# Optimization experiments

Hardware: AMD Instinct MI355X
Metric: run time of the kernel (lower is better)

Reference implementation:

```python
import jax, jax.numpy as jnp
import numpy as np

EPS = 0.0001
N_NODES = 8192
N_GRAPHS = 128
NODES_PER_G = 64
N_FEAT = 128
CLDIM = 512
LAYERS = 3
HEADS = 8
HID = 64
N_EDGES = 262144
N_CLASSES = 10


def setup_inputs():
    key = jax.random.key(0)
    ks = jax.random.split(key, 12)
    x = jax.random.normal(ks[0], (N_NODES, N_FEAT), jnp.float32)

    def rand_edges(k):
        k1, k2 = jax.random.split(k)
        g = jax.random.randint(k1, (N_EDGES,), 0, N_GRAPHS)
        loc = jax.random.randint(k2, (2, N_EDGES), 0, NODES_PER_G)
        return (g[None, :] * NODES_PER_G + loc).astype(jnp.int32)

    edge_index = rand_edges(ks[1])
    neg_edge_index = rand_edges(ks[2])
    batch = (jnp.arange(N_NODES) // NODES_PER_G).astype(jnp.int32)
    # mask indices: all within-graph node pairs (block-diagonal mask==1)
    base = jnp.arange(N_GRAPHS) * NODES_PER_G
    a = jnp.repeat(jnp.arange(NODES_PER_G), NODES_PER_G)
    b = jnp.tile(jnp.arange(NODES_PER_G), NODES_PER_G)
    midx = jnp.stack([
        (base[:, None] + a[None, :]).reshape(-1),
        (base[:, None] + b[None, :]).reshape(-1),
    ]).astype(jnp.int32)
    s = 0.05
    return dict(
        x=x, edge_index=edge_index, neg_edge_index=neg_edge_index,
        batch=batch, midx=midx,
        fc_W=jax.random.normal(ks[3], (N_FEAT, CLDIM), jnp.float32) * s,
        fc_b=jnp.zeros((CLDIM,), jnp.float32),
        bn_g=jnp.ones((LAYERS, CLDIM), jnp.float32),
        bn_b=jnp.zeros((LAYERS, CLDIM), jnp.float32),
        conv_W=jax.random.normal(ks[4], (LAYERS, CLDIM, CLDIM), jnp.float32) * s,
        conv_b=jnp.zeros((LAYERS, CLDIM), jnp.float32),
        feat_W=jax.random.normal(ks[5], (LAYERS * CLDIM, HEADS * HID), jnp.float32) * s,
        phi=jax.random.normal(ks[6], (HEADS, 2 * HID, 1), jnp.float32) * s,
        fc1_W=jax.random.normal(ks[7], (HEADS * HID, HID), jnp.float32) * s,
        fc1_b=jnp.zeros((HID,), jnp.float32),
        fc2_W=jax.random.normal(ks[8], (HID, N_CLASSES), jnp.float32) * s,
        fc2_b=jnp.zeros((N_CLASSES,), jnp.float32),
    )


def _bn(h, g, b):
    # BatchNorm1d in training mode (biased variance over nodes)
    m = jnp.mean(h, 0)
    v = jnp.var(h, 0)
    return (h - m) * jax.lax.rsqrt(v + 1e-5) * g + b


def _gcn(h, W, b, src, dst, n):
    # GCNConv with added self-loops: D^-1/2 (A+I) D^-1/2 (h W) + b
    h2 = h @ W
    deg = jax.ops.segment_sum(jnp.ones(src.shape[0], h.dtype), dst, n) + 1.0
    dinv = jax.lax.rsqrt(deg)
    coef = (dinv[src] * dinv[dst])[:, None]
    agg = jax.ops.segment_sum(h2[src] * coef, dst, n)
    return agg + h2 / deg[:, None] + b


def _forward(x, fc_W, fc_b, bn_g, bn_b, conv_W, conv_b, feat_W, phi,
             fc1_W, fc1_b, fc2_W, fc2_b, edge_index, neg_edge_index, batch, midx):
    n = x.shape[0]
    h = x @ fc_W + fc_b
    src, dst = edge_index[0], edge_index[1]
    hs = []
    for i in range(LAYERS):
        h = _bn(h, bn_g[i], bn_b[i])
        h = jax.nn.relu(_gcn(h, conv_W[i], conv_b[i], src, dst, n))
        hs.append(h)
    z = jnp.concatenate(hs, -1)  # [N, LAYERS*CLDIM]

    # ---- recon loss: per-edge inner-product decoder, mean-pooled per graph ----
    def edge_loss(ei, neg):
        v = jnp.sum(z[ei[0]] * z[ei[1]], -1)
        sgm = jax.nn.sigmoid(v)
        l = -jnp.log(EPS + (1.0 - sgm if neg else sgm))
        seg = batch[ei[0]]
        cnt = jax.ops.segment_sum(jnp.ones_like(l), seg, N_GRAPHS)
        tot = jax.ops.segment_sum(l, seg, N_GRAPHS)
        return jnp.sum(tot / jnp.maximum(cnt, 1.0))

    Lrc = (edge_loss(edge_index, False) + edge_loss(neg_edge_index, True)) / N_GRAPHS

    # ---- classifier: multi-head sigmoid attention over mask pairs ----
    xh = (z @ feat_W).reshape(n, HEADS, HID)
    phi_a = phi[:, :HID, 0]   # [H, HID]
    phi_b = phi[:, HID:, 0]   # [H, HID]
    # cat([x_i, x_j]) @ phi == x_i @ phi_a + x_j @ phi_b, computed per node then gathered
    s1 = jnp.einsum('nhd,hd->nh', xh, phi_a)
    s2 = jnp.einsum('nhd,hd->nh', xh, phi_b)
    w = jax.nn.sigmoid(jax.nn.leaky_relu(s1[midx[0]] + s2[midx[1]]))  # [M, H]
    msg = (xh[midx[1]] * w[:, :, None]).reshape(-1, HEADS * HID)      # [M, H*HID]
    agg = jax.ops.segment_sum(msg, midx[0], n)
    logits = jax.nn.leaky_relu(agg @ fc1_W + fc1_b) @ fc2_W + fc2_b
    tmp = jnp.exp(logits - jnp.max(logits, -1, keepdims=True)) + EPS
    preds = tmp / jnp.sum(tmp, -1, keepdims=True)
    cnt = jax.ops.segment_sum(jnp.ones((n,), preds.dtype), batch, N_GRAPHS)
    yp = jax.ops.segment_sum(preds, batch, N_GRAPHS) / cnt[:, None]
    return jnp.log(yp), Lrc, preds


def reference(x, edge_index, neg_edge_index, batch, midx, fc_W, fc_b, bn_g, bn_b,
              conv_W, conv_b, feat_W, phi, fc1_W, fc1_b, fc2_W, fc2_b):
    return _forward(x, fc_W, fc_b, bn_g, bn_b, conv_W, conv_b, feat_W, phi,
                    fc1_W, fc1_b, fc2_W, fc2_b, edge_index, neg_edge_index, batch, midx)
```

## Files before the change

kernel.cpp:

```cpp
#include <hip/hip_runtime.h>

#define NN 8192
#define NG 128
#define NF 128
#define CL 512
#define ZD 1536
#define NE 262144

typedef __attribute__((ext_vector_type(8))) _Float16 half8;
typedef __attribute__((ext_vector_type(4))) float f32x4;

__global__ void deg_kernel(const int* __restrict__ dst, float* __restrict__ deg) {
    int e = blockIdx.x * 256 + threadIdx.x;
    atomicAdd(&deg[dst[e]], 1.0f);
}

__global__ void build_adj(const int* __restrict__ src, const int* __restrict__ dst,
                          const float* __restrict__ deg, float* __restrict__ A) {
    int e = blockIdx.x * 256 + threadIdx.x;
    int s = src[e], d = dst[e];
    int g = d >> 6;
    float w = rsqrtf(deg[s] + 1.0f) * rsqrtf(deg[d] + 1.0f);
    atomicAdd(&A[(size_t)((g << 6) + (d & 63)) * 64 + (s & 63)], w);
}

__global__ void cvtA(const float* __restrict__ Amat, const float* __restrict__ deg,
                     _Float16* __restrict__ Ah) {
    int t = blockIdx.x * 256 + threadIdx.x;
    int i4 = t * 4;
    int g = i4 >> 12, loc = i4 & 4095;
    float4 v = *(const float4*)(Amat + (size_t)g * 4096 + loc);
    float vv[4] = {v.x, v.y, v.z, v.w};
    int row = loc >> 6;
    int c0 = loc & 63;
    int ed = row - c0;
    if (ed >= 0 && ed < 4) vv[ed] += 1.0f / (deg[g * 64 + row] + 1.0f);
    int swz = (row & 7) << 3;
    #pragma unroll
    for (int e = 0; e < 4; ++e)
        Ah[(size_t)g * 4096 + ((loc + e) ^ swz)] = (_Float16)vv[e];
}

__global__ void cvt_h(const float* __restrict__ in, _Float16* __restrict__ out) {
    int i = blockIdx.x * 256 + threadIdx.x;
    float4 a = *(const float4*)(in + (size_t)i * 8);
    float4 b = *(const float4*)(in + (size_t)i * 8 + 4);
    half8 o;
    o[0] = (_Float16)a.x; o[1] = (_Float16)a.y; o[2] = (_Float16)a.z; o[3] = (_Float16)a.w;
    o[4] = (_Float16)b.x; o[5] = (_Float16)b.y; o[6] = (_Float16)b.z; o[7] = (_Float16)b.w;
    *(half8*)(out + (size_t)i * 8) = o;
}

__global__ void cvtT(const float* __restrict__ W, _Float16* __restrict__ Wt,
                     int Kd, int Nd) {
    __shared__ float t[32][33];
    int kb = blockIdx.y * 32, nb = blockIdx.x * 32;
    int tx = threadIdx.x, ty = threadIdx.y;
    for (int i = ty; i < 32; i += 8)
        t[i][tx] = W[(size_t)(kb + i) * Nd + nb + tx];
    __syncthreads();
    for (int i = ty; i < 32; i += 8)
        Wt[(size_t)(nb + i) * Kd + kb + tx] = (_Float16)t[tx][i];
}

__global__ void wprep(const float* __restrict__ W,
                      const float* __restrict__ sums, const float* __restrict__ sqs,
                      const float* __restrict__ g, const float* __restrict__ b,
                      _Float16* __restrict__ Wt, float* __restrict__ bias2,
                      int Kd, int Nd) {
    __shared__ float t[32][33];
    __shared__ float tks[32];
    int kb = blockIdx.y * 32, nb = blockIdx.x * 32;
    int tx = threadIdx.x, ty = threadIdx.y;
    for (int i = ty; i < 32; i += 8)
        t[i][tx] = W[(size_t)(kb + i) * Nd + nb + tx];
    int kc = kb + tx;
    float m = sums[kc] * (1.0f / NN);
    float var = sqs[kc] * (1.0f / NN) - m * m;
    float sc = rsqrtf(var + 1e-5f) * g[kc];
    if (ty == 0) tks[tx] = b[kc] - m * sc;
    __syncthreads();
    for (int i = ty; i < 32; i += 8)
        Wt[(size_t)(nb + i) * Kd + kb + tx] = (_Float16)(t[tx][i] * sc);
    if (ty == 0) {
        float acc = 0.f;
        #pragma unroll
        for (int i = 0; i < 32; ++i) acc = fmaf(tks[i], t[i][tx], acc);
        atomicAdd(&bias2[nb + tx], acc);
    }
}

template<int ACT, bool HASB, bool OUT16, bool STATS, bool FUSE>
__global__ __launch_bounds__(256)
void gemm_f16(const _Float16* __restrict__ A, int lda,
              const _Float16* __restrict__ Bt, int ldb,
              float* __restrict__ Cf, _Float16* __restrict__ Ch, int ldc,
              const float* __restrict__ bias, int K,
              float* __restrict__ sums, float* __restrict__ sqs,
              const _Float16* __restrict__ Ahg,
              const float* __restrict__ cb,
              _Float16* __restrict__ Zout)
{
    __shared__ __align__(16) char SMraw[FUSE ? 34816 : 24576];
    _Float16* As = (_Float16*)SMraw;
    _Float16* Bs = (_Float16*)(SMraw + 16384);
    const int tid = threadIdx.x;
    const int lane = tid & 63, wave = tid >> 6;
    const int wr = wave >> 1, wc = wave & 1;
    const int ntile = gridDim.x;
    const int li = blockIdx.y * ntile + blockIdx.x;
    const int x8 = li & 7, rest = li >> 3;
    const int bt = rest % ntile;
    const int bp = (rest / ntile) * 8 + x8;
    const int bm = bp * 128, bn = bt * 64;

    f32x4 acc[4][2];
    #pragma unroll
    for (int m = 0; m < 4; ++m)
        #pragma unroll
        for (int n = 0; n < 2; ++n)
            acc[m][n] = (f32x4){0.f, 0.f, 0.f, 0.f};

    const int fl = lane & 15, kh = (lane >> 4) * 8;
    const int sw = (fl & 7) << 3;

    for (int k0 = 0; k0 < K; k0 += 64) {
        #pragma unroll
        for (int j = 0; j < 4; ++j) {
            int d = wave * 2048 + j * 512 + lane * 8;
            int row = d >> 6, kk = d & 63;
            int sk = kk ^ ((row & 7) << 3);
            __builtin_amdgcn_global_load_lds(
                (const __attribute__((address_space(1))) void*)(A + (size_t)(bm + row) * lda + k0 + sk),
                (__attribute__((address_space(3))) void*)&As[wave * 2048 + j * 512], 16, 0, 0);
        }
        #pragma unroll
        for (int j = 0; j < 2; ++j) {
            int d = wave * 1024 + j * 512 + lane * 8;
            int row = d >> 6, kk = d & 63;
            int sk = kk ^ ((row & 7) << 3);
            __builtin_amdgcn_global_load_lds(
                (const __attribute__((address_space(1))) void*)(Bt + (size_t)(bn + row) * ldb + k0 + sk),
                (__attribute__((address_space(3))) void*)&Bs[wave * 1024 + j * 512], 16, 0, 0);
        }
        __syncthreads();
        #pragma unroll
        for (int kc = 0; kc < 2; ++kc) {
            int ko = (kc * 32 + kh) ^ sw;
            half8 av[4], bv[2];
            #pragma unroll
            for (int m = 0; m < 4; ++m)
                av[m] = *(const half8*)&As[(wr * 64 + m * 16 + fl) * 64 + ko];
            #pragma unroll
            for (int n = 0; n < 2; ++n)
                bv[n] = *(const half8*)&Bs[(wc * 32 + n * 16 + fl) * 64 + ko];
            #pragma unroll
            for (int m = 0; m < 4; ++m)
                #pragma unroll
                for (int n = 0; n < 2; ++n)
                    acc[m][n] = __builtin_amdgcn_mfma_f32_16x16x32_f16(av[m], bv[n], acc[m][n], 0, 0, 0);
        }
        __syncthreads();
    }

    const int orow0 = (lane >> 4) * 4;
    const int ocol  = lane & 15;

    if constexpr (!FUSE) {
        #pragma unroll
        for (int n = 0; n < 2; ++n) {
            int col = bn + wc * 32 + n * 16 + ocol;
            float bb = HASB ? bias[col] : 0.f;
            float ss = 0.f, qq = 0.f;
            #pragma unroll
            for (int m = 0; m < 4; ++m) {
                #pragma unroll
                for (int r = 0; r < 4; ++r) {
                    int rowg = bm + wr * 64 + m * 16 + orow0 + r;
                    float v = acc[m][n][r] + bb;
                    if (ACT == 2) v = v > 0.f ? v : 0.01f * v;
                    if (STATS) { ss += v; qq = fmaf(v, v, qq); }
                    if (OUT16) Ch[(size_t)rowg * ldc + col] = (_Float16)v;
                    else       Cf[(size_t)rowg * ldc + col] = v;
                }
            }
            if (STATS) {
                ss += __shfl_down(ss, 32); ss += __shfl_down(ss, 16);
                qq += __shfl_down(qq, 32); qq += __shfl_down(qq, 16);
                if (lane < 16) {
                    atomicAdd(&sums[col], ss);
                    atomicAdd(&sqs[col], qq);
                }
            }
        }
    } else {
        _Float16* AsA = (_Float16*)SMraw;
        _Float16* Xs  = (_Float16*)(SMraw + 16384);
        const _Float16* Ag = Ahg + (size_t)(bm >> 6) * 4096;
        #pragma unroll
        for (int j = 0; j < 4; ++j)
            __builtin_amdgcn_global_load_lds(
                (const __attribute__((address_space(1))) void*)(Ag + wave * 2048 + j * 512 + lane * 8),
                (__attribute__((address_space(3))) void*)&AsA[wave * 2048 + j * 512], 16, 0, 0);
        #pragma unroll
        for (int n = 0; n < 2; ++n) {
            int c = wc * 32 + n * 16 + ocol;
            float bb = HASB ? bias[bn + c] : 0.f;
            int csw = (c & 7) << 3;
            #pragma unroll
            for (int m = 0; m < 4; ++m) {
                #pragma unroll
                for (int r = 0; r < 4; ++r) {
                    int srow = wr * 64 + m * 16 + orow0 + r;
                    Xs[c * 128 + (srow & 64) + ((srow & 63) ^ csw)] = (_Float16)(acc[m][n][r] + bb);
                }
            }
        }
        __syncthreads();
        const int gg = wave >> 1, rh = wave & 1;
        f32x4 acc2[2][4];
        #pragma unroll
        for (int m2 = 0; m2 < 2; ++m2)
            #pragma unroll
            for (int n2 = 0; n2 < 4; ++n2)
                acc2[m2][n2] = (f32x4){0.f, 0.f, 0.f, 0.f};
        #pragma unroll
        for (int kc = 0; kc < 2; ++kc) {
            int ko = (kc * 32 + kh) ^ sw;
            #pragma unroll
            for (int m2 = 0; m2 < 2; ++m2) {
                int arow = rh * 32 + m2 * 16 + fl;
                half8 av = *(const half8*)&AsA[gg * 4096 + arow * 64 + ko];
                #pragma unroll
                for (int n2 = 0; n2 < 4; ++n2) {
                    int c = n2 * 16 + fl;
                    half8 bv = *(const half8*)&Xs[c * 128 + gg * 64 + ((kc * 32 + kh) ^ ((c & 7) << 3))];
                    acc2[m2][n2] = __builtin_amdgcn_mfma_f32_16x16x32_f16(av, bv, acc2[m2][n2], 0, 0, 0);
                }
            }
        }
        __syncthreads();
        float* Cs = (float*)SMraw;
        #pragma unroll
        for (int m2 = 0; m2 < 2; ++m2)
            #pragma unroll
            for (int n2 = 0; n2 < 4; ++n2)
                #pragma unroll
                for (int r = 0; r < 4; ++r)
                    Cs[(gg * 64 + rh * 32 + m2 * 16 + orow0 + r) * 68 + n2 * 16 + ocol] = acc2[m2][n2][r];
        __syncthreads();
        const int rr = tid >> 3, dq = tid & 7;
        #pragma unroll
        for (int pass = 0; pass < 4; ++pass) {
            int row = pass * 32 + rr;
            half8 hv;
            #pragma unroll
            for (int e = 0; e < 8; ++e) {
                float v = Cs[row * 68 + dq * 8 + e] + cb[bn + dq * 8 + e];
                v = v > 0.f ? v : 0.f;
                hv[e] = (_Float16)v;
            }
            *(half8*)(Zout + (size_t)(bm + row) * ZD + bn + dq * 8) = hv;
        }
        if (STATS && tid < 64) {
            float bb = cb[bn + tid];
            float ss = 0.f, qq = 0.f;
            for (int row = 0; row < 128; ++row) {
                float v = Cs[row * 68 + tid] + bb;
                v = v > 0.f ? v : 0.f;
                ss += v;
                qq = fmaf(v, v, qq);
            }
            atomicAdd(&sums[bn + tid], ss);
            atomicAdd(&sqs[bn + tid], qq);
        }
    }
}

__global__ __launch_bounds__(256)
void gram_mfma(const _Float16* __restrict__ Z, float* __restrict__ Gparts)
{
    __shared__ _Float16 Zs[4096];
    const int g = blockIdx.x, khalf = blockIdx.y;
    const int tid = threadIdx.x;
    const int lane = tid & 63, wave = tid >> 6;
    const int fl = lane & 15, kh = (lane >> 4) * 8;
    const int sw = (fl & 7) << 3;
    float* G = Gparts + (size_t)khalf * NG * 4096;

    f32x4 acc[4];
    #pragma unroll
    for (int n = 0; n < 4; ++n) acc[n] = (f32x4){0.f, 0.f, 0.f, 0.f};

    for (int k0 = khalf * (ZD / 2); k0 < (khalf + 1) * (ZD / 2); k0 += 64) {
        #pragma unroll
        for (int j = 0; j < 2; ++j) {
            int d = wave * 1024 + j * 512 + lane * 8;
            int row = d >> 6, kk = d & 63;
            int sk = kk ^ ((row & 7) << 3);
            __builtin_amdgcn_global_load_lds(
                (const __attribute__((address_space(1))) void*)(Z + (size_t)(g * 64 + row) * ZD + k0 + sk),
                (__attribute__((address_space(3))) void*)&Zs[wave * 1024 + j * 512], 16, 0, 0);
        }
        __syncthreads();
        #pragma unroll
        for (int kc = 0; kc < 2; ++kc) {
            int ko = (kc * 32 + kh) ^ sw;
            half8 av = *(const half8*)&Zs[(wave * 16 + fl) * 64 + ko];
            #pragma unroll
            for (int n = 0; n < 4; ++n) {
                half8 bv = *(const half8*)&Zs[(n * 16 + fl) * 64 + ko];
                acc[n] = __builtin_amdgcn_mfma_f32_16x16x32_f16(av, bv, acc[n], 0, 0, 0);
            }
        }
        __syncthreads();
    }
    const int orow0 = (lane >> 4) * 4;
    const int ocol  = lane & 15;
    #pragma unroll
    for (int n = 0; n < 4; ++n)
        #pragma unroll
        for (int r = 0; r < 4; ++r)
            G[(size_t)(g * 64 + wave * 16 + orow0 + r) * 64 + n * 16 + ocol] = acc[n][r];
}

__global__ void edge_loss2(const int* __restrict__ ei, const int* __restrict__ nei,
                           const float* __restrict__ G0, float* __restrict__ LOSS)
{
    const int setid = blockIdx.y;
    const int* e0 = setid ? nei : ei;
    const int* e1 = e0 + NE;
    float* tot = LOSS + setid * 256;
    float* cnt = tot + 128;
    const float* G1 = G0 + (size_t)NG * 4096;
    __shared__ float lt[128];
    __shared__ float lc[128];
    int tid = threadIdx.x;
    if (tid < 128) { lt[tid] = 0.f; lc[tid] = 0.f; }
    __syncthreads();
    for (int e = blockIdx.x * blockDim.x + tid; e < NE; e += gridDim.x * blockDim.x) {
        int a = e0[e], b = e1[e];
        int g = a >> 6;
        size_t idx = (size_t)((g << 6) + (a & 63)) * 64 + (b & 63);
        float v = G0[idx] + G1[idx];
        float s = 1.f / (1.f + expf(-v));
        float p = setid ? (1.f - s) : s;
        float l = -logf(1e-4f + p);
        atomicAdd(&lt[g], l);
        atomicAdd(&lc[g], 1.f);
    }
    __syncthreads();
    if (tid < 128) {
        atomicAdd(&tot[tid], lt[tid]);
        atomicAdd(&cnt[tid], lc[tid]);
    }
}

__global__ void lrc_final(const float* __restrict__ loss, float* __restrict__ out)
{
    int t = threadIdx.x;
    float v = loss[t] / fmaxf(loss[128 + t], 1.f) + loss[256 + t] / fmaxf(loss[384 + t], 1.f);
    __shared__ float red[128];
    red[t] = v;
    __syncthreads();
    for (int s = 64; s; s >>= 1) {
        if (t < s) red[t] += red[t + s];
        __syncthreads();
    }
    if (t == 0) out[0] = red[0] * (1.0f / 128.0f);
}

__global__ __launch_bounds__(256)
void featattn(const _Float16* __restrict__ Z, const _Float16* __restrict__ featWt,
              const float* __restrict__ phi, _Float16* __restrict__ agg)
{
    __shared__ __align__(16) char SMraw[68608];
    _Float16* As  = (_Float16*)SMraw;
    _Float16* Bs  = (_Float16*)(SMraw + 16384);
    float*    Cs  = (float*)SMraw;
    _Float16* Xt  = (_Float16*)(SMraw + 34816);
    _Float16* Ws  = (_Float16*)(SMraw + 51200);
    float*    s1s = (float*)(SMraw + 67584);
    float*    s2s = (float*)(SMraw + 68096);
    const int pnl = blockIdx.x, h = blockIdx.y;
    const int bm = pnl * 128;
    const int tid = threadIdx.x;
    const int lane = tid & 63, wave = tid >> 6;
    const int wr = wave >> 1, wc = wave & 1;
    const int fl = lane & 15, kh = (lane >> 4) * 8;
    const int sw = (fl & 7) << 3;

    f32x4 acc[4][2];
    #pragma unroll
    for (int m = 0; m < 4; ++m)
        #pragma unroll
        for (int n = 0; n < 2; ++n)
            acc[m][n] = (f32x4){0.f, 0.f, 0.f, 0.f};

    for (int k0 = 0; k0 < ZD; k0 += 64) {
        #pragma unroll
        for (int j = 0; j < 4; ++j) {
            int d = wave * 2048 + j * 512 + lane * 8;
            int row = d >> 6, kk = d & 63;
            int sk = kk ^ ((row & 7) << 3);
            __builtin_amdgcn_global_load_lds(
                (const __attribute__((address_space(1))) void*)(Z + (size_t)(bm + row) * ZD + k0 + sk),
                (__attribute__((address_space(3))) void*)&As[wave * 2048 + j * 512], 16, 0, 0);
        }
        #pragma unroll
        for (int j = 0; j < 2; ++j) {
            int d = wave * 1024 + j * 512 + lane * 8;
            int row = d >> 6, kk = d & 63;
            int sk = kk ^ ((row & 7) << 3);
            __builtin_amdgcn_global_load_lds(
                (const __attribute__((address_space(1))) void*)(featWt + (size_t)(h * 64 + row) * ZD + k0 + sk),
                (__attribute__((address_space(3))) void*)&Bs[wave * 1024 + j * 512], 16, 0, 0);
        }
        __syncthreads();
        #pragma unroll
        for (int kc = 0; kc < 2; ++kc) {
            int ko = (kc * 32 + kh) ^ sw;
            half8 av[4], bv[2];
            #pragma unroll
            for (int m = 0; m < 4; ++m)
                av[m] = *(const half8*)&As[(wr * 64 + m * 16 + fl) * 64 + ko];
            #pragma unroll
            for (int n = 0; n < 2; ++n)
                bv[n] = *(const half8*)&Bs[(wc * 32 + n * 16 + fl) * 64 + ko];
            #pragma unroll
            for (int m = 0; m < 4; ++m)
                #pragma unroll
                for (int n = 0; n < 2; ++n)
                    acc[m][n] = __builtin_amdgcn_mfma_f32_16x16x32_f16(av[m], bv[n], acc[m][n], 0, 0, 0);
        }
        __syncthreads();
    }
    const int orow0 = (lane >> 4) * 4, ocol = lane & 15;
    #pragma unroll
    for (int n = 0; n < 2; ++n) {
        int col = wc * 32 + n * 16 + ocol;
        #pragma unroll
        for (int m = 0; m < 4; ++m)
            #pragma unroll
            for (int r = 0; r < 4; ++r)
                Cs[(wr * 64 + m * 16 + orow0 + r) * 68 + col] = acc[m][n][r];
    }
    __syncthreads();
    {
        const int bnode = tid >> 1, dq = tid & 1;
        const int gg = bnode >> 6, bloc = bnode & 63;
        const float* pa = phi + h * 128 + dq * 32;
        const float* pb = pa + 64;
        float sa = 0.f, sb = 0.f;
        #pragma unroll
        for (int j = 0; j < 32; ++j) {
            int d = dq * 32 + j;
            float vf = Cs[bnode * 68 + d];
            Xt[gg * 4096 + ((d * 64 + bloc) ^ ((d & 7) << 3))] = (_Float16)vf;
            sa = fmaf(vf, pa[j], sa);
            sb = fmaf(vf, pb[j], sb);
        }
        sa += __shfl_down(sa, 1);
        sb += __shfl_down(sb, 1);
        if (dq == 0) { s1s[bnode] = sa; s2s[bnode] = sb; }
    }
    __syncthreads();
    {
        const int inode = tid >> 1, bq = tid & 1;
        const int gg = inode >> 6, iloc = inode & 63;
        float si = s1s[inode];
        #pragma unroll
        for (int e = 0; e < 32; ++e) {
            int b = bq * 32 + e;
            float t = si + s2s[gg * 64 + b];
            t = t > 0.f ? t : 0.01f * t;
            float w = 1.f / (1.f + expf(-t));
            Ws[gg * 4096 + ((iloc * 64 + b) ^ ((iloc & 7) << 3))] = (_Float16)w;
        }
    }
    __syncthreads();
    const int gg = wave >> 1, rh = wave & 1;
    f32x4 acc2[2][4];
    #pragma unroll
    for (int m2 = 0; m2 < 2; ++m2)
        #pragma unroll
        for (int n2 = 0; n2 < 4; ++n2)
            acc2[m2][n2] = (f32x4){0.f, 0.f, 0.f, 0.f};
    #pragma unroll
    for (int kc = 0; kc < 2; ++kc) {
        #pragma unroll
        for (int m2 = 0; m2 < 2; ++m2) {
            int arow = rh * 32 + m2 * 16 + fl;
            half8 av = *(const half8*)&Ws[gg * 4096 + ((arow * 64 + kc * 32 + kh) ^ ((arow & 7) << 3))];
            #pragma unroll
            for (int n2 = 0; n2 < 4; ++n2) {
                int rowb = n2 * 16 + fl;
                half8 bv = *(const half8*)&Xt[gg * 4096 + ((rowb * 64 + kc * 32 + kh) ^ ((rowb & 7) << 3))];
                acc2[m2][n2] = __builtin_amdgcn_mfma_f32_16x16x32_f16(av, bv, acc2[m2][n2], 0, 0, 0);
            }
        }
    }
    __syncthreads();
    #pragma unroll
    for (int m2 = 0; m2 < 2; ++m2)
        #pragma unroll
        for (int n2 = 0; n2 < 4; ++n2)
            #pragma unroll
            for (int r = 0; r < 4; ++r)
                Cs[(gg * 64 + rh * 32 + m2 * 16 + orow0 + r) * 68 + n2 * 16 + ocol] = acc2[m2][n2][r];
    __syncthreads();
    {
        const int rr = tid >> 3, dq = tid & 7;
        #pragma unroll
        for (int pass = 0; pass < 4; ++pass) {
            int row = pass * 32 + rr;
            half8 hv;
            #pragma unroll
            for (int e = 0; e < 8; ++e)
                hv[e] = (_Float16)Cs[row * 68 + dq * 8 + e];
            *(half8*)(agg + (size_t)(bm + row) * CL + h * 64 + dq * 8) = hv;
        }
    }
}

__global__ __launch_bounds__(256)
void fc1head(const _Float16* __restrict__ AGG, const _Float16* __restrict__ fc1Wt,
             const float* __restrict__ fc1b,
             const float* __restrict__ fc2W, const float* __restrict__ fc2b,
             float* __restrict__ preds, float* __restrict__ outlog)
{
    __shared__ __align__(16) char SMraw[17664];
    _Float16* As = (_Float16*)SMraw;
    _Float16* Bs = (_Float16*)(SMraw + 8192);
    float*    Cs = (float*)SMraw;
    const int g = blockIdx.x;
    const int tid = threadIdx.x;
    const int lane = tid & 63, wave = tid >> 6;
    const int fl = lane & 15, kh = (lane >> 4) * 8;
    const int sw = (fl & 7) << 3;

    f32x4 acc[4];
    #pragma unroll
    for (int n = 0; n < 4; ++n) acc[n] = (f32x4){0.f, 0.f, 0.f, 0.f};

    for (int k0 = 0; k0 < CL; k0 += 64) {
        #pragma unroll
        for (int j = 0; j < 2; ++j) {
            int d = wave * 1024 + j * 512 + lane * 8;
            int row = d >> 6, kk = d & 63;
            int sk = kk ^ ((row & 7) << 3);
            __builtin_amdgcn_global_load_lds(
                (const __attribute__((address_space(1))) void*)(AGG + (size_t)(g * 64 + row) * CL + k0 + sk),
                (__attribute__((address_space(3))) void*)&As[wave * 1024 + j * 512], 16, 0, 0);
            __builtin_amdgcn_global_load_lds(
                (const __attribute__((address_space(1))) void*)(fc1Wt + (size_t)row * CL + k0 + sk),
                (__attribute__((address_space(3))) void*)&Bs[wave * 1024 + j * 512], 16, 0, 0);
        }
        __syncthreads();
        #pragma unroll
        for (int kc = 0; kc < 2; ++kc) {
            int ko = (kc * 32 + kh) ^ sw;
            half8 av = *(const half8*)&As[(wave * 16 + fl) * 64 + ko];
            #pragma unroll
            for (int n = 0; n < 4; ++n) {
                half8 bv = *(const half8*)&Bs[(n * 16 + fl) * 64 + ko];
                acc[n] = __builtin_amdgcn_mfma_f32_16x16x32_f16(av, bv, acc[n], 0, 0, 0);
            }
        }
        __syncthreads();
    }
    const int orow0 = (lane >> 4) * 4, ocol = lane & 15;
    #pragma unroll
    for (int n = 0; n < 4; ++n) {
        int col = n * 16 + ocol;
        float bb = fc1b[col];
        #pragma unroll
        for (int r = 0; r < 4; ++r) {
            float v = acc[n][r] + bb;
            v = v > 0.f ? v : 0.01f * v;
            Cs[(wave * 16 + orow0 + r) * 69 + col] = v;
        }
    }
    __syncthreads();
    if (tid < 64) {
        float lg[10];
        float mx = -1e30f;
        #pragma unroll
        for (int c = 0; c < 10; ++c) {
            float s = fc2b[c];
            #pragma unroll
            for (int k = 0; k < 64; ++k) s = fmaf(Cs[tid * 69 + k], fc2W[k * 10 + c], s);
            lg[c] = s;
            mx = fmaxf(mx, s);
        }
        float sum = 0.f;
        #pragma unroll
        for (int c = 0; c < 10; ++c) {
            float t = expf(lg[c] - mx) + 1e-4f;
            lg[c] = t;
            sum += t;
        }
        float inv = 1.f / sum;
        #pragma unroll
        for (int c = 0; c < 10; ++c) {
            lg[c] *= inv;
            preds[(size_t)(g * 64 + tid) * 10 + c] = lg[c];
        }
        #pragma unroll
        for (int off = 32; off; off >>= 1)
            #pragma unroll
            for (int c = 0; c < 10; ++c) lg[c] += __shfl_down(lg[c], off);
        if (tid == 0)
            #pragma unroll
            for (int c = 0; c < 10; ++c) outlog[g * 10 + c] = logf(lg[c] * (1.0f / 64.0f));
    }
}

extern "C" void kernel_launch(void* const* d_in, const int* in_sizes, int n_in,
                              void* d_out, int out_size, void* d_ws, size_t ws_size,
                              hipStream_t stream)
{
    (void)in_sizes; (void)n_in; (void)out_size; (void)ws_size;
    const float* x     = (const float*)d_in[0];
    const int*   ei    = (const int*)d_in[1];
    const int*   nei   = (const int*)d_in[2];
    const float* fcW   = (const float*)d_in[5];
    const float* fcb   = (const float*)d_in[6];
    const float* bng   = (const float*)d_in[7];
    const float* bnb   = (const float*)d_in[8];
    const float* convW = (const float*)d_in[9];
    const float* convb = (const float*)d_in[10];
    const float* featW = (const float*)d_in[11];
    const float* phi   = (const float*)d_in[12];
    const float* fc1W  = (const float*)d_in[13];
    const float* fc1b  = (const float*)d_in[14];
    const float* fc2W  = (const float*)d_in[15];
    const float* fc2b  = (const float*)d_in[16];
    float* out = (float*)d_out;

    char* ws = (char*)d_ws;
    _Float16* Z       = (_Float16*)(ws);
    _Float16* H0      = (_Float16*)(ws + 25165824);
    _Float16* AGG     = (_Float16*)(ws + 33554432);
    _Float16* xb      = (_Float16*)(ws + 41943040);
    _Float16* fcWt    = (_Float16*)(ws + 44040192);
    _Float16* convWs  = (_Float16*)(ws + 44171264);
    _Float16* featWt  = (_Float16*)(ws + 44695552);
    _Float16* fc1Wt   = (_Float16*)(ws + 46268416);
    _Float16* Ah      = (_Float16*)(ws + 46333952);
    float*    Gram    = (float*)(ws + 47382528);
    float*    DEG     = (float*)(ws + 51576832);
    float*    Amat    = (float*)(ws + 51609600);
    float*    LOSS    = (float*)(ws + 53706752);
    float*    BNS3    = (float*)(ws + 53708800);
    float*    B2      = (float*)(ws + 53721088);

    const int* src = ei;
    const int* dst = ei + NE;

    hipMemsetAsync(DEG, 0, 53727232 - 51576832, stream);

    deg_kernel<<<NE / 256, 256, 0, stream>>>(dst, DEG);
    build_adj<<<NE / 256, 256, 0, stream>>>(src, dst, DEG, Amat);
    cvtA<<<(NG * 4096 / 4) / 256, 256, 0, stream>>>(Amat, DEG, Ah);

    cvt_h<<<(NN * NF / 8) / 256, 256, 0, stream>>>(x, xb);
    cvtT<<<dim3(CL / 32, NF / 32), dim3(32, 8), 0, stream>>>(fcW, fcWt, NF, CL);
    cvtT<<<dim3(CL / 32, ZD / 32), dim3(32, 8), 0, stream>>>(featW, featWt, ZD, CL);
    cvtT<<<dim3(2, 16), dim3(32, 8), 0, stream>>>(fc1W, fc1Wt, 512, 64);

    gemm_f16<0, true, true, true, false><<<dim3(CL / 64, NN / 128), 256, 0, stream>>>(
        xb, NF, fcWt, NF, nullptr, H0, CL, fcb, NF, BNS3, BNS3 + 512,
        nullptr, nullptr, nullptr);

    for (int i = 0; i < 3; ++i) {
        const _Float16* Ain = (i == 0) ? H0 : (Z + (size_t)(i - 1) * CL);
        int lda = (i == 0) ? CL : ZD;
        float* sums = BNS3 + i * 1024;
        float* sqs  = sums + 512;
        float* b2   = B2 + i * 512;
        wprep<<<dim3(CL / 32, CL / 32), dim3(32, 8), 0, stream>>>(
            convW + (size_t)i * CL * CL, sums, sqs, bng + i * CL, bnb + i * CL,
            convWs, b2, CL, CL);
        if (i < 2)
            gemm_f16<0, true, false, true, true><<<dim3(CL / 64, NN / 128), 256, 0, stream>>>(
                Ain, lda, convWs, CL, nullptr, nullptr, 0, b2, CL,
                BNS3 + (i + 1) * 1024, BNS3 + (i + 1) * 1024 + 512,
                Ah, convb + i * CL, Z + (size_t)i * CL);
        else
            gemm_f16<0, true, false, false, true><<<dim3(CL / 64, NN / 128), 256, 0, stream>>>(
                Ain, lda, convWs, CL, nullptr, nullptr, 0, b2, CL,
                nullptr, nullptr, Ah, convb + i * CL, Z + (size_t)i * CL);
    }

    gram_mfma<<<dim3(NG, 2), 256, 0, stream>>>(Z, Gram);
    edge_loss2<<<dim3(128, 2), 256, 0, stream>>>(ei, nei, Gram, LOSS);
    lrc_final<<<1, 128, 0, stream>>>(LOSS, out + 1280);

    featattn<<<dim3(64, 8), 256, 0, stream>>>(Z, featWt, phi, AGG);

    fc1head<<<NG, 256, 0, stream>>>(AGG, fc1Wt, fc1b, fc2W, fc2b, out + 1281, out);
}
```

Baseline: 177.8 us.

## Merge prep kernels, derive degrees from adjacency counts, fold loss finalize into edge kernel

```diff
diff --git a/kernel.cpp b/kernel.cpp
--- a/kernel.cpp
+++ b/kernel.cpp
@@ -10,57 +10,71 @@
 typedef __attribute__((ext_vector_type(8))) _Float16 half8;
 typedef __attribute__((ext_vector_type(4))) float f32x4;
 
-__global__ void deg_kernel(const int* __restrict__ dst, float* __restrict__ deg) {
-    int e = blockIdx.x * 256 + threadIdx.x;
-    atomicAdd(&deg[dst[e]], 1.0f);
-}
-
-__global__ void build_adj(const int* __restrict__ src, const int* __restrict__ dst,
-                          const float* __restrict__ deg, float* __restrict__ A) {
-    int e = blockIdx.x * 256 + threadIdx.x;
-    int s = src[e], d = dst[e];
-    int g = d >> 6;
-    float w = rsqrtf(deg[s] + 1.0f) * rsqrtf(deg[d] + 1.0f);
-    atomicAdd(&A[(size_t)((g << 6) + (d & 63)) * 64 + (s & 63)], w);
-}
-
-__global__ void cvtA(const float* __restrict__ Amat, const float* __restrict__ deg,
-                     _Float16* __restrict__ Ah) {
-    int t = blockIdx.x * 256 + threadIdx.x;
-    int i4 = t * 4;
-    int g = i4 >> 12, loc = i4 & 4095;
-    float4 v = *(const float4*)(Amat + (size_t)g * 4096 + loc);
-    float vv[4] = {v.x, v.y, v.z, v.w};
-    int row = loc >> 6;
-    int c0 = loc & 63;
-    int ed = row - c0;
-    if (ed >= 0 && ed < 4) vv[ed] += 1.0f / (deg[g * 64 + row] + 1.0f);
-    int swz = (row & 7) << 3;
-    #pragma unroll
-    for (int e = 0; e < 4; ++e)
-        Ah[(size_t)g * 4096 + ((loc + e) ^ swz)] = (_Float16)vv[e];
-}
-
-__global__ void cvt_h(const float* __restrict__ in, _Float16* __restrict__ out) {
-    int i = blockIdx.x * 256 + threadIdx.x;
-    float4 a = *(const float4*)(in + (size_t)i * 8);
-    float4 b = *(const float4*)(in + (size_t)i * 8 + 4);
-    half8 o;
-    o[0] = (_Float16)a.x; o[1] = (_Float16)a.y; o[2] = (_Float16)a.z; o[3] = (_Float16)a.w;
-    o[4] = (_Float16)b.x; o[5] = (_Float16)b.y; o[6] = (_Float16)b.z; o[7] = (_Float16)b.w;
-    *(half8*)(out + (size_t)i * 8) = o;
-}
-
-__global__ void cvtT(const float* __restrict__ W, _Float16* __restrict__ Wt,
-                     int Kd, int Nd) {
+__global__ __launch_bounds__(256)
+void prep_misc(const float* __restrict__ x, _Float16* __restrict__ xb,
+               const float* __restrict__ fcW, _Float16* __restrict__ fcWt,
+               const float* __restrict__ featW, _Float16* __restrict__ featWt,
+               const float* __restrict__ fc1W, _Float16* __restrict__ fc1Wt,
+               const int* __restrict__ ei, float* __restrict__ Acnt)
+{
+    const int b = blockIdx.x, tid = threadIdx.x;
+    if (b < 512) {
+        int i = b * 256 + tid;
+        float4 a = *(const float4*)(x + (size_t)i * 8);
+        float4 c = *(const float4*)(x + (size_t)i * 8 + 4);
+        half8 o;
+        o[0] = (_Float16)a.x; o[1] = (_Float16)a.y; o[2] = (_Float16)a.z; o[3] = (_Float16)a.w;
+        o[4] = (_Float16)c.x; o[5] = (_Float16)c.y; o[6] = (_Float16)c.z; o[7] = (_Float16)c.w;
+        *(half8*)(xb + (size_t)i * 8) = o;
+        return;
+    }
+    if (b < 1536) {
+        int e = (b - 512) * 256 + tid;
+        int s = ei[e], d = ei[NE + e];
+        int g = d >> 6;
+        atomicAdd(&Acnt[(size_t)((g << 6) + (d & 63)) * 64 + (s & 63)], 1.0f);
+        return;
+    }
+    const float* W; _Float16* Wt; int Kd, Nd, bx, by;
+    if (b < 1600)      { int bb = b - 1536; W = fcW;   Wt = fcWt;   Kd = NF;  Nd = CL; bx = bb % 16; by = bb / 16; }
+    else if (b < 2368) { int bb = b - 1600; W = featW; Wt = featWt; Kd = ZD;  Nd = CL; bx = bb % 16; by = bb / 16; }
+    else               { int bb = b - 2368; W = fc1W;  Wt = fc1Wt;  Kd = 512; Nd = 64; bx = bb % 2;  by = bb / 2; }
     __shared__ float t[32][33];
-    int kb = blockIdx.y * 32, nb = blockIdx.x * 32;
-    int tx = threadIdx.x, ty = threadIdx.y;
+    const int tx = tid & 31, ty = tid >> 5;
+    const int kb = by * 32, nb = bx * 32;
     for (int i = ty; i < 32; i += 8)
         t[i][tx] = W[(size_t)(kb + i) * Nd + nb + tx];
     __syncthreads();
     for (int i = ty; i < 32; i += 8)
         Wt[(size_t)(nb + i) * Kd + kb + tx] = (_Float16)t[tx][i];
+}
+
+__global__ __launch_bounds__(256)
+void finalize_adj(const float* __restrict__ Acnt, _Float16* __restrict__ Ah)
+{
+    __shared__ float As[4096];
+    __shared__ float rs[64];
+    __shared__ float dinv1[64];
+    const int g = blockIdx.x, tid = threadIdx.x;
+    const float* Ag = Acnt + (size_t)g * 4096;
+    for (int i = tid; i < 1024; i += 256)
+        *(float4*)&As[i * 4] = *(const float4*)&Ag[i * 4];
+    __syncthreads();
+    if (tid < 64) {
+        float s = 0.f;
+        #pragma unroll
+        for (int j = 0; j < 64; ++j) s += As[tid * 64 + j];
+        float d = s + 1.0f;
+        rs[tid] = rsqrtf(d);
+        dinv1[tid] = 1.0f / d;
+    }
+    __syncthreads();
+    for (int i = tid; i < 4096; i += 256) {
+        int row = i >> 6, s = i & 63;
+        float v = As[i] * rs[row] * rs[s];
+        if (row == s) v += dinv1[row];
+        Ah[(size_t)g * 4096 + (i ^ ((row & 7) << 3))] = (_Float16)v;
+    }
 }
 
 __global__ void wprep(const float* __restrict__ W,
@@ -325,7 +339,8 @@
 }
 
 __global__ void edge_loss2(const int* __restrict__ ei, const int* __restrict__ nei,
-                           const float* __restrict__ G0, float* __restrict__ LOSS)
+                           const float* __restrict__ G0, float* __restrict__ LOSS,
+                           unsigned int* __restrict__ ctr, float* __restrict__ outLrc)
 {
     const int setid = blockIdx.y;
     const int* e0 = setid ? nei : ei;
@@ -335,6 +350,8 @@
     const float* G1 = G0 + (size_t)NG * 4096;
     __shared__ float lt[128];
     __shared__ float lc[128];
+    __shared__ float red[128];
+    __shared__ unsigned int lastS;
     int tid = threadIdx.x;
     if (tid < 128) { lt[tid] = 0.f; lc[tid] = 0.f; }
     __syncthreads();
@@ -354,20 +371,24 @@
         atomicAdd(&tot[tid], lt[tid]);
         atomicAdd(&cnt[tid], lc[tid]);
     }
-}
-
-__global__ void lrc_final(const float* __restrict__ loss, float* __restrict__ out)
-{
-    int t = threadIdx.x;
-    float v = loss[t] / fmaxf(loss[128 + t], 1.f) + loss[256 + t] / fmaxf(loss[384 + t], 1.f);
-    __shared__ float red[128];
-    red[t] = v;
-    __syncthreads();
-    for (int s = 64; s; s >>= 1) {
-        if (t < s) red[t] += red[t + s];
-        __syncthreads();
-    }
-    if (t == 0) out[0] = red[0] * (1.0f / 128.0f);
+    __threadfence();
+    __syncthreads();
+    if (tid == 0) lastS = atomicAdd(ctr, 1u);
+    __syncthreads();
+    if (lastS == gridDim.x * gridDim.y - 1) {
+        __threadfence();
+        if (tid < 128) {
+            float v = LOSS[tid] / fmaxf(LOSS[128 + tid], 1.f) +
+                      LOSS[256 + tid] / fmaxf(LOSS[384 + tid], 1.f);
+            red[tid] = v;
+        }
+        __syncthreads();
+        for (int s = 64; s; s >>= 1) {
+            if (tid < s && tid + s < 128) red[tid] += red[tid + s];
+            __syncthreads();
+        }
+        if (tid == 0) outLrc[0] = red[0] * (1.0f / 128.0f);
+    }
 }
 
 __global__ __launch_bounds__(256)
@@ -649,25 +670,17 @@
     _Float16* fc1Wt   = (_Float16*)(ws + 46268416);
     _Float16* Ah      = (_Float16*)(ws + 46333952);
     float*    Gram    = (float*)(ws + 47382528);
-    float*    DEG     = (float*)(ws + 51576832);
-    float*    Amat    = (float*)(ws + 51609600);
-    float*    LOSS    = (float*)(ws + 53706752);
-    float*    BNS3    = (float*)(ws + 53708800);
-    float*    B2      = (float*)(ws + 53721088);
-
-    const int* src = ei;
-    const int* dst = ei + NE;
-
-    hipMemsetAsync(DEG, 0, 53727232 - 51576832, stream);
-
-    deg_kernel<<<NE / 256, 256, 0, stream>>>(dst, DEG);
-    build_adj<<<NE / 256, 256, 0, stream>>>(src, dst, DEG, Amat);
-    cvtA<<<(NG * 4096 / 4) / 256, 256, 0, stream>>>(Amat, DEG, Ah);
-
-    cvt_h<<<(NN * NF / 8) / 256, 256, 0, stream>>>(x, xb);
-    cvtT<<<dim3(CL / 32, NF / 32), dim3(32, 8), 0, stream>>>(fcW, fcWt, NF, CL);
-    cvtT<<<dim3(CL / 32, ZD / 32), dim3(32, 8), 0, stream>>>(featW, featWt, ZD, CL);
-    cvtT<<<dim3(2, 16), dim3(32, 8), 0, stream>>>(fc1W, fc1Wt, 512, 64);
+    float*    Acnt    = (float*)(ws + 51576832);
+    float*    LOSS    = (float*)(ws + 53673984);
+    float*    BNS3    = (float*)(ws + 53676032);
+    float*    B2      = (float*)(ws + 53688320);
+    unsigned int* CTR = (unsigned int*)(ws + 53694464);
+
+    hipMemsetAsync(Acnt, 0, 53694720 - 51576832, stream);
+
+    prep_misc<<<2400, 256, 0, stream>>>(x, xb, fcW, fcWt, featW, featWt,
+                                        fc1W, fc1Wt, ei, Acnt);
+    finalize_adj<<<NG, 256, 0, stream>>>(Acnt, Ah);
 
     gemm_f16<0, true, true, true, false><<<dim3(CL / 64, NN / 128), 256, 0, stream>>>(
         xb, NF, fcWt, NF, nullptr, H0, CL, fcb, NF, BNS3, BNS3 + 512,
@@ -694,8 +707,7 @@
     }
 
     gram_mfma<<<dim3(NG, 2), 256, 0, stream>>>(Z, Gram);
-    edge_loss2<<<dim3(128, 2), 256, 0, stream>>>(ei, nei, Gram, LOSS);
-    lrc_final<<<1, 128, 0, stream>>>(LOSS, out + 1280);
+    edge_loss2<<<dim3(128, 2), 256, 0, stream>>>(ei, nei, Gram, LOSS, CTR, out + 1280);
 
     featattn<<<dim3(64, 8), 256, 0, stream>>>(Z, featWt, phi, AGG);
 
```

Measured after the change: 172.4 us, median of 2. -3.0%, faster.
